# Performance work log

Measured on AMD Instinct MI355X. Metric: run time of the kernel, lower is better.

The kernel has to match this reference:

```python
import jax, jax.numpy as jnp
import numpy as np

W_H = 512
RING_WIDTH = 1
IN_F = 128
OUT_F = 128


def _ring_ids():
    # static ring assignment per pixel, mirrors torch module's self.r / ring_width bins
    ax = np.arange(-W_H / 2, W_H / 2, dtype=np.float64)
    x, y = np.meshgrid(ax, ax, indexing='ij')
    r = np.sqrt(x * x + y * y)
    ring = (r // RING_WIDTH).astype(np.int32).reshape(-1)  # [H*W]
    len_r = int(np.sqrt(2.0) * (W_H / 2)) + 1
    iter_r = len_r // RING_WIDTH + (1 if len_r % RING_WIDTH != 0 else 0)
    return jnp.asarray(ring), iter_r


def setup_inputs() -> dict:
    key = jax.random.key(0)
    ks = jax.random.split(key, 7)
    return {
        'image_re': jax.random.normal(ks[0], (W_H, W_H, IN_F), jnp.float32),
        'image_im': jax.random.normal(ks[1], (W_H, W_H, IN_F), jnp.float32),
        'mask': jax.random.randint(ks[2], (W_H, W_H), 0, 2).astype(jnp.int32),
        'output_re': jnp.zeros((W_H, W_H, OUT_F), jnp.float32),
        'output_im': jnp.zeros((W_H, W_H, OUT_F), jnp.float32),
        'w1_re': jax.random.normal(ks[3], (IN_F, OUT_F), jnp.float32),
        'w1_im': jax.random.normal(ks[4], (IN_F, OUT_F), jnp.float32),
        'w2_re': jax.random.normal(ks[5], (IN_F, OUT_F), jnp.float32),
        'w2_im': jax.random.normal(ks[6], (IN_F, OUT_F), jnp.float32),
    }


def reference(image_re, image_im, mask, output_re, output_im,
              w1_re, w1_im, w2_re, w2_im):
    ring, n_rings = _ring_ids()
    H, _, F_in = image_re.shape
    x_re = image_re.reshape(-1, F_in)  # [N, F_in]
    x_im = image_im.reshape(-1, F_in)
    m = mask.reshape(-1, 1)
    u = (m == 0).astype(x_re.dtype)  # uncorrupted indicator
    c = (m == 1).astype(x_re.dtype)  # corrupted indicator

    # uncor complex matmul (x*u) @ W1, as 4 real GEMMs
    xu_re, xu_im = x_re * u, x_im * u
    mm1_re = xu_re @ w1_re - xu_im @ w1_im
    mm1_im = xu_re @ w1_im + xu_im @ w1_re

    # per-ring mean of mm1 (denominator = full ring size, matching neighbor.shape[0])
    counts = jax.ops.segment_sum(jnp.ones((x_re.shape[0],), x_re.dtype), ring,
                                 num_segments=n_rings)
    denom = jnp.maximum(counts, 1.0)[:, None]
    sum_re = jax.ops.segment_sum(mm1_re, ring, num_segments=n_rings) / denom
    sum_im = jax.ops.segment_sum(mm1_im, ring, num_segments=n_rings) / denom
    sre = sum_re[ring]  # [N, F_out] per-pixel broadcast of its ring mean
    sim = sum_im[ring]

    # cor complex matmul (x*c) @ W2
    xc_re, xc_im = x_re * c, x_im * c
    mm2_re = xc_re @ w2_re - xc_im @ w2_im
    mm2_im = xc_re @ w2_im + xc_im @ w2_re

    out_re = u * (0.5 * (mm1_re + sre)) + c * (mm2_re - sre)
    out_im = u * (0.5 * (mm1_im + sim)) + c * (mm2_im - sim)
    # real/imag stacked on last axis -> [H, H, F_out, 2]
    return jnp.stack([out_re, out_im], axis=-1).reshape(H, H, -1, 2)
```

## Files before the change

### kernel.cpp

```cpp
#include <hip/hip_runtime.h>
#include <hip/hip_bf16.h>
#include <stdint.h>


#define WH 512
#define NPIX (WH * WH)
#define NF 128
#define NRINGS 363
#define SLAB 1664

typedef unsigned short u16;
typedef __attribute__((ext_vector_type(8))) short short8;
typedef __attribute__((ext_vector_type(4))) float floatx4;

__device__ __forceinline__ u16 f2bf(float x) {
    uint32_t u = __float_as_uint(x);
    uint32_t r = (u + 0x7FFFu + ((u >> 16) & 1u)) >> 16;
    return (u16)r;
}
__device__ __forceinline__ uint32_t pk(float a, float b) {
    return (uint32_t)f2bf(a) | ((uint32_t)f2bf(b) << 16);
}
__device__ __forceinline__ short8 negbf(short8 v) {
    union { short8 s; uint32_t u[4]; } x;
    x.s = v;
    x.u[0] ^= 0x80008000u; x.u[1] ^= 0x80008000u;
    x.u[2] ^= 0x80008000u; x.u[3] ^= 0x80008000u;
    return x.s;
}
__device__ __forceinline__ floatx4 mfma16(short8 a, short8 b, floatx4 c) {
    return __builtin_amdgcn_mfma_f32_16x16x32_bf16(a, b, c, 0, 0, 0);
}
__device__ __forceinline__ int ring_of(int p) {
    int i = p >> 9, j = p & 511;
    int x = i - 256, y = j - 256;
    int r2 = x * x + y * y;
    int R = (int)sqrtf((float)r2);
    while ((R + 1) * (R + 1) <= r2) R++;
    while (R * R > r2) R--;
    return R;
}

__global__ void k_build_bt(const float* __restrict__ w1r, const float* __restrict__ w1i,
                           const float* __restrict__ w2r, const float* __restrict__ w2i,
                           u16* __restrict__ bt) {
    int n = blockIdx.x, k = threadIdx.x;
    int src = k * NF + n;
    float a1r = w1r[src], a1i = w1i[src], a2r = w2r[src], a2i = w2i[src];
    int d = n * NF + k;
    bt[0 * 16384 + d] = f2bf(a1r - a2r);
    bt[1 * 16384 + d] = f2bf(a2r);
    bt[2 * 16384 + d] = f2bf(a1i - a2i);
    bt[3 * 16384 + d] = f2bf(a2i);
}

__global__ void k_scatter(const int* __restrict__ mask, int* __restrict__ ctr,
                          int* __restrict__ totcnt, int* __restrict__ list)
{
    int p = blockIdx.x * 256 + threadIdx.x;
    int R = ring_of(p);
    atomicAdd(&totcnt[R], 1);
    if (mask[p] == 0) {
        int slot = atomicAdd(&ctr[R], 1);
        list[R * SLAB + slot] = p;
    }
}

__global__ __launch_bounds__(256) void k_xsum(
    const float* __restrict__ xr, const float* __restrict__ xi,
    const int* __restrict__ ctr, const int* __restrict__ list,
    float* __restrict__ xsum)
{
    const int R = blockIdx.x;
    const int nu = ctr[R];
    const int s0 = blockIdx.y * 128;
    if (s0 >= nu) return;
    const int n = min(128, nu - s0);
    __shared__ int sl[128];
    const int t = threadIdx.x;
    if (t < 128) sl[t] = (t < n) ? list[R * SLAB + s0 + t] : 0;
    __syncthreads();
    const float* src = (t < 128) ? xr : xi;
    const int col = t & 127;
    float acc = 0.0f;
#pragma unroll 4
    for (int k = 0; k < n; k++) {
        int p = sl[k];
        acc += src[(size_t)p * NF + col];
    }
    atomicAdd(&xsum[R * 256 + t], acc);
}

__global__ __launch_bounds__(256) void k_smean(
    const float* __restrict__ xsum, const int* __restrict__ totcnt,
    const float* __restrict__ w1r, const float* __restrict__ w1i,
    float* __restrict__ smean)
{
    const int R = blockIdx.x;
    const int t = threadIdx.x;
    const int f = t & 127, part = t >> 7;
    __shared__ float sh[256];
    sh[t] = xsum[R * 256 + t];
    __syncthreads();
    float acc = 0.0f;
#pragma unroll 4
    for (int k = 0; k < NF; k++) {
        float ar = sh[k], ai = sh[128 + k];
        float br = w1r[k * NF + f], bi = w1i[k * NF + f];
        acc += part ? (ar * bi + ai * br) : (ar * br - ai * bi);
    }
    float c = (float)totcnt[R];
    c = (c < 1.0f) ? 1.0f : c;
    smean[R * 256 + f * 2 + part] = acc / c;
}

#define BROW 40
#define LDS_AR 0
#define LDS_AI 5120
#define LDS_B  10240

__global__ __launch_bounds__(256, 2) void k_gemm(
    const float* __restrict__ xr, const float* __restrict__ xi,
    const int* __restrict__ mask, const u16* __restrict__ bt,
    const float* __restrict__ smean, float* __restrict__ out)
{
    __shared__ u16 lds[30720];
    const int t = threadIdx.x;
    const int pbase = blockIdx.x * 128;
    const int w = t >> 6, lane = t & 63;
    const int quad = lane >> 4, l16 = lane & 15;

    floatx4 accRe[2][8], accIm[2][8];
#pragma unroll
    for (int mi = 0; mi < 2; mi++)
#pragma unroll
        for (int ni = 0; ni < 8; ni++) {
            accRe[mi][ni] = (floatx4)0.0f;
            accIm[mi][ni] = (floatx4)0.0f;
        }

    bool uu[2];
    uu[0] = (mask[pbase + w * 32 + l16] == 0);
    uu[1] = (mask[pbase + w * 32 + 16 + l16] == 0);

    const int sr = t >> 1, sh = t & 1;
    const float4* xr4 = (const float4*)(xr + (size_t)(pbase + sr) * NF);
    const float4* xi4 = (const float4*)(xi + (size_t)(pbase + sr) * NF);

    for (int kw = 0; kw < 4; kw++) {
        if (kw) __syncthreads();
        {
            int qb = kw * 8 + sh * 4;
            float4 r0 = xr4[qb], r1 = xr4[qb + 1], r2 = xr4[qb + 2], r3 = xr4[qb + 3];
            float4 i0 = xi4[qb], i1 = xi4[qb + 1], i2 = xi4[qb + 2], i3 = xi4[qb + 3];
            uint4 a, b;
            a.x = pk(r0.x, r0.y); a.y = pk(r0.z, r0.w); a.z = pk(r1.x, r1.y); a.w = pk(r1.z, r1.w);
            b.x = pk(r2.x, r2.y); b.y = pk(r2.z, r2.w); b.z = pk(r3.x, r3.y); b.w = pk(r3.z, r3.w);
            *(uint4*)&lds[LDS_AR + sr * BROW + sh * 16]     = a;
            *(uint4*)&lds[LDS_AR + sr * BROW + sh * 16 + 8] = b;
            a.x = pk(i0.x, i0.y); a.y = pk(i0.z, i0.w); a.z = pk(i1.x, i1.y); a.w = pk(i1.z, i1.w);
            b.x = pk(i2.x, i2.y); b.y = pk(i2.z, i2.w); b.z = pk(i3.x, i3.y); b.w = pk(i3.z, i3.w);
            *(uint4*)&lds[LDS_AI + sr * BROW + sh * 16]     = a;
            *(uint4*)&lds[LDS_AI + sr * BROW + sh * 16 + 8] = b;
        }
#pragma unroll
        for (int q = 0; q < 8; q++) {
            int fi = q * 256 + t;
            int mat = fi >> 9;
            int wi = fi & 511;
            int n = wi >> 2, kc = wi & 3;
            uint4 v = *(const uint4*)(bt + mat * 16384 + n * 128 + kw * 32 + kc * 8);
            *(uint4*)&lds[LDS_B + mat * 5120 + n * BROW + kc * 8] = v;
        }
        __syncthreads();

        short8 ar[2], ai[2], aru[2], aiu[2];
#pragma unroll
        for (int mi = 0; mi < 2; mi++) {
            int r = w * 32 + mi * 16 + l16;
            ar[mi] = *(short8*)&lds[LDS_AR + r * BROW + quad * 8];
            ai[mi] = *(short8*)&lds[LDS_AI + r * BROW + quad * 8];
            aru[mi] = uu[mi] ? ar[mi] : (short8)0;
            aiu[mi] = uu[mi] ? ai[mi] : (short8)0;
        }
#pragma unroll
        for (int ni = 0; ni < 8; ni++) {
            int nrow = ni * 16 + l16;
            short8 bDr = *(short8*)&lds[LDS_B + 0 * 5120 + nrow * BROW + quad * 8];
            short8 b2r = *(short8*)&lds[LDS_B + 1 * 5120 + nrow * BROW + quad * 8];
            short8 bDi = *(short8*)&lds[LDS_B + 2 * 5120 + nrow * BROW + quad * 8];
            short8 b2i = *(short8*)&lds[LDS_B + 3 * 5120 + nrow * BROW + quad * 8];
            short8 bDin = negbf(bDi), b2in = negbf(b2i);
#pragma unroll
            for (int mi = 0; mi < 2; mi++) {
                accRe[mi][ni] = mfma16(aru[mi], bDr,  accRe[mi][ni]);
                accRe[mi][ni] = mfma16(ar[mi],  b2r,  accRe[mi][ni]);
                accRe[mi][ni] = mfma16(aiu[mi], bDin, accRe[mi][ni]);
                accRe[mi][ni] = mfma16(ai[mi],  b2in, accRe[mi][ni]);
                accIm[mi][ni] = mfma16(aru[mi], bDi,  accIm[mi][ni]);
                accIm[mi][ni] = mfma16(ar[mi],  b2i,  accIm[mi][ni]);
                accIm[mi][ni] = mfma16(aiu[mi], bDr,  accIm[mi][ni]);
                accIm[mi][ni] = mfma16(ai[mi],  b2r,  accIm[mi][ni]);
            }
        }
    }

    int  Rp[2][4];
    bool up[2][4];
#pragma unroll
    for (int mi = 0; mi < 2; mi++)
#pragma unroll
        for (int r = 0; r < 4; r++) {
            int p = pbase + w * 32 + mi * 16 + quad * 4 + r;
            Rp[mi][r] = ring_of(p);
            up[mi][r] = (mask[p] == 0);
        }
#pragma unroll
    for (int mi = 0; mi < 2; mi++)
#pragma unroll
        for (int ni = 0; ni < 8; ni++)
#pragma unroll
            for (int r = 0; r < 4; r++) {
                int p = pbase + w * 32 + mi * 16 + quad * 4 + r;
                int f = ni * 16 + l16;
                float2 sv = *(const float2*)(smean + (size_t)Rp[mi][r] * 256 + f * 2);
                float vre = accRe[mi][ni][r];
                float vim = accIm[mi][ni][r];
                float2 o;
                if (up[mi][r]) { o.x = 0.5f * (vre + sv.x); o.y = 0.5f * (vim + sv.y); }
                else           { o.x = vre - sv.x;          o.y = vim - sv.y; }
                *(float2*)(out + (size_t)p * 256 + f * 2) = o;
            }
}

extern "C" void kernel_launch(void* const* d_in, const int* in_sizes, int n_in,
                              void* d_out, int out_size, void* d_ws, size_t ws_size,
                              hipStream_t stream)
{
    const float* xr  = (const float*)d_in[0];
    const float* xi  = (const float*)d_in[1];
    const int*   msk = (const int*)d_in[2];
    const float* w1r = (const float*)d_in[5];
    const float* w1i = (const float*)d_in[6];
    const float* w2r = (const float*)d_in[7];
    const float* w2i = (const float*)d_in[8];
    float* out = (float*)d_out;

    char* wsb = (char*)d_ws;
    float* xsum   = (float*)(wsb + 0);
    float* smean  = (float*)(wsb + 371712);
    int*   ctr    = (int*)(wsb + 743424);
    int*   totcnt = (int*)(wsb + 744960);
    int*   list   = (int*)(wsb + 746496);
    u16*   bt     = (u16*)(wsb + 3162624);

    hipMemsetAsync(d_ws, 0, 746496, stream);
    k_build_bt<<<dim3(128), dim3(128), 0, stream>>>(w1r, w1i, w2r, w2i, bt);
    k_scatter<<<dim3(NPIX / 256), dim3(256), 0, stream>>>(msk, ctr, totcnt, list);
    k_xsum<<<dim3(NRINGS, 13), dim3(256), 0, stream>>>(xr, xi, ctr, list, xsum);
    k_smean<<<dim3(NRINGS), dim3(256), 0, stream>>>(xsum, totcnt, w1r, w1i, smean);
    k_gemm<<<dim3(NPIX / 128), dim3(256), 0, stream>>>(xr, xi, msk, bt, smean, out);
}
```

Measured before the change: 796.1 us.

## Prefetch A tiles, DMA pre-laid-out B to LDS, vectorize ring x-sum

```diff
diff --git a/kernel.cpp b/kernel.cpp
--- a/kernel.cpp
+++ b/kernel.cpp
@@ -30,6 +30,11 @@
 }
 __device__ __forceinline__ floatx4 mfma16(short8 a, short8 b, floatx4 c) {
     return __builtin_amdgcn_mfma_f32_16x16x32_bf16(a, b, c, 0, 0, 0);
+}
+__device__ __forceinline__ void dma16(const void* gsrc, void* ldst) {
+    __builtin_amdgcn_global_load_lds(
+        (const __attribute__((address_space(1))) void*)gsrc,
+        (__attribute__((address_space(3))) void*)ldst, 16, 0, 0);
 }
 __device__ __forceinline__ int ring_of(int p) {
     int i = p >> 9, j = p & 511;
@@ -41,17 +46,19 @@
     return R;
 }
 
+#define BROW 40
 __global__ void k_build_bt(const float* __restrict__ w1r, const float* __restrict__ w1i,
                            const float* __restrict__ w2r, const float* __restrict__ w2i,
                            u16* __restrict__ bt) {
     int n = blockIdx.x, k = threadIdx.x;
     int src = k * NF + n;
     float a1r = w1r[src], a1i = w1i[src], a2r = w2r[src], a2i = w2i[src];
-    int d = n * NF + k;
-    bt[0 * 16384 + d] = f2bf(a1r - a2r);
-    bt[1 * 16384 + d] = f2bf(a2r);
-    bt[2 * 16384 + d] = f2bf(a1i - a2i);
-    bt[3 * 16384 + d] = f2bf(a2i);
+    int kw = k >> 5, kl = k & 31;
+    size_t d = (size_t)kw * 20480 + (size_t)n * BROW + kl;
+    bt[d + 0 * 5120] = f2bf(a1r - a2r);
+    bt[d + 1 * 5120] = f2bf(a2r);
+    bt[d + 2 * 5120] = f2bf(a1i - a2i);
+    bt[d + 3 * 5120] = f2bf(a2i);
 }
 
 __global__ void k_scatter(const int* __restrict__ mask, int* __restrict__ ctr,
@@ -77,18 +84,30 @@
     if (s0 >= nu) return;
     const int n = min(128, nu - s0);
     __shared__ int sl[128];
+    __shared__ float4 red4[256];
     const int t = threadIdx.x;
     if (t < 128) sl[t] = (t < n) ? list[R * SLAB + s0 + t] : 0;
     __syncthreads();
-    const float* src = (t < 128) ? xr : xi;
-    const int col = t & 127;
-    float acc = 0.0f;
+    const float* src = (t & 128) ? xi : xr;
+    const int c4 = t & 31;
+    const int j = (t >> 5) & 3;
+    float4 acc = {0.0f, 0.0f, 0.0f, 0.0f};
 #pragma unroll 4
-    for (int k = 0; k < n; k++) {
+    for (int k = j; k < n; k += 4) {
         int p = sl[k];
-        acc += src[(size_t)p * NF + col];
-    }
-    atomicAdd(&xsum[R * 256 + t], acc);
+        float4 v = *(const float4*)(src + (size_t)p * NF + c4 * 4);
+        acc.x += v.x; acc.y += v.y; acc.z += v.z; acc.w += v.w;
+    }
+    red4[t] = acc;
+    __syncthreads();
+    if ((t & 96) == 0) {
+        float4 a0 = red4[t], a1 = red4[t + 32], a2 = red4[t + 64], a3 = red4[t + 96];
+        int base = R * 256 + ((t >> 7) & 1) * 128 + c4 * 4;
+        atomicAdd(&xsum[base + 0], a0.x + a1.x + a2.x + a3.x);
+        atomicAdd(&xsum[base + 1], a0.y + a1.y + a2.y + a3.y);
+        atomicAdd(&xsum[base + 2], a0.z + a1.z + a2.z + a3.z);
+        atomicAdd(&xsum[base + 3], a0.w + a1.w + a2.w + a3.w);
+    }
 }
 
 __global__ __launch_bounds__(256) void k_smean(
@@ -114,7 +133,6 @@
     smean[R * 256 + f * 2 + part] = acc / c;
 }
 
-#define BROW 40
 #define LDS_AR 0
 #define LDS_AI 5120
 #define LDS_B  10240
@@ -147,32 +165,52 @@
     const float4* xr4 = (const float4*)(xr + (size_t)(pbase + sr) * NF);
     const float4* xi4 = (const float4*)(xi + (size_t)(pbase + sr) * NF);
 
+    float4 pr[4], pi[4];
+    {
+        int qb = sh * 4;
+        pr[0] = xr4[qb]; pr[1] = xr4[qb + 1]; pr[2] = xr4[qb + 2]; pr[3] = xr4[qb + 3];
+        pi[0] = xi4[qb]; pi[1] = xi4[qb + 1]; pi[2] = xi4[qb + 2]; pi[3] = xi4[qb + 3];
+    }
+
     for (int kw = 0; kw < 4; kw++) {
-        if (kw) __syncthreads();
+        if (kw) {
+            __builtin_amdgcn_s_barrier();
+            __builtin_amdgcn_sched_barrier(0);
+            asm volatile("" ::: "memory");
+        }
         {
-            int qb = kw * 8 + sh * 4;
-            float4 r0 = xr4[qb], r1 = xr4[qb + 1], r2 = xr4[qb + 2], r3 = xr4[qb + 3];
-            float4 i0 = xi4[qb], i1 = xi4[qb + 1], i2 = xi4[qb + 2], i3 = xi4[qb + 3];
+            const char* src = (const char*)bt + (size_t)kw * 40960 + w * 10240 + lane * 16;
+            u16* dst = &lds[LDS_B + w * 5120];
+#pragma unroll
+            for (int c = 0; c < 10; c++)
+                dma16(src + c * 1024, dst + c * 512);
+        }
+        asm volatile("s_waitcnt vmcnt(10)" ::: "memory");
+        {
             uint4 a, b;
-            a.x = pk(r0.x, r0.y); a.y = pk(r0.z, r0.w); a.z = pk(r1.x, r1.y); a.w = pk(r1.z, r1.w);
-            b.x = pk(r2.x, r2.y); b.y = pk(r2.z, r2.w); b.z = pk(r3.x, r3.y); b.w = pk(r3.z, r3.w);
+            a.x = pk(pr[0].x, pr[0].y); a.y = pk(pr[0].z, pr[0].w);
+            a.z = pk(pr[1].x, pr[1].y); a.w = pk(pr[1].z, pr[1].w);
+            b.x = pk(pr[2].x, pr[2].y); b.y = pk(pr[2].z, pr[2].w);
+            b.z = pk(pr[3].x, pr[3].y); b.w = pk(pr[3].z, pr[3].w);
             *(uint4*)&lds[LDS_AR + sr * BROW + sh * 16]     = a;
             *(uint4*)&lds[LDS_AR + sr * BROW + sh * 16 + 8] = b;
-            a.x = pk(i0.x, i0.y); a.y = pk(i0.z, i0.w); a.z = pk(i1.x, i1.y); a.w = pk(i1.z, i1.w);
-            b.x = pk(i2.x, i2.y); b.y = pk(i2.z, i2.w); b.z = pk(i3.x, i3.y); b.w = pk(i3.z, i3.w);
+            a.x = pk(pi[0].x, pi[0].y); a.y = pk(pi[0].z, pi[0].w);
+            a.z = pk(pi[1].x, pi[1].y); a.w = pk(pi[1].z, pi[1].w);
+            b.x = pk(pi[2].x, pi[2].y); b.y = pk(pi[2].z, pi[2].w);
+            b.z = pk(pi[3].x, pi[3].y); b.w = pk(pi[3].z, pi[3].w);
             *(uint4*)&lds[LDS_AI + sr * BROW + sh * 16]     = a;
             *(uint4*)&lds[LDS_AI + sr * BROW + sh * 16 + 8] = b;
         }
-#pragma unroll
-        for (int q = 0; q < 8; q++) {
-            int fi = q * 256 + t;
-            int mat = fi >> 9;
-            int wi = fi & 511;
-            int n = wi >> 2, kc = wi & 3;
-            uint4 v = *(const uint4*)(bt + mat * 16384 + n * 128 + kw * 32 + kc * 8);
-            *(uint4*)&lds[LDS_B + mat * 5120 + n * BROW + kc * 8] = v;
-        }
-        __syncthreads();
+        asm volatile("s_waitcnt vmcnt(0)" ::: "memory");
+        if (kw < 3) {
+            int qb = (kw + 1) * 8 + sh * 4;
+            pr[0] = xr4[qb]; pr[1] = xr4[qb + 1]; pr[2] = xr4[qb + 2]; pr[3] = xr4[qb + 3];
+            pi[0] = xi4[qb]; pi[1] = xi4[qb + 1]; pi[2] = xi4[qb + 2]; pi[3] = xi4[qb + 3];
+        }
+        asm volatile("s_waitcnt lgkmcnt(0)" ::: "memory");
+        __builtin_amdgcn_s_barrier();
+        __builtin_amdgcn_sched_barrier(0);
+        asm volatile("" ::: "memory");
 
         short8 ar[2], ai[2], aru[2], aiu[2];
 #pragma unroll
```

Result: faster. 775.6 us (-2.6%).
